# Kernel tuning notes

Hardware: AMD Instinct MI355X
Metric: run time of the kernel (lower is better)

## Reference

```python
import jax, jax.numpy as jnp
import numpy as np
import math

B, H, S, D = 2, 16, 2048, 128

def setup_inputs() -> dict:
    key = jax.random.key(0)
    k1, k2, k3, k4 = jax.random.split(key, 4)
    x1 = jax.random.normal(k1, (B, H, S, D), dtype=jnp.float32)
    x2 = jax.random.normal(k2, (B, H, S, D), dtype=jnp.float32)
    x3 = jax.random.normal(k3, (B, H, D, S), dtype=jnp.float32)
    attn_mask = jax.random.normal(k4, (S, S), dtype=jnp.float32)
    return {"x1": x1, "x2": x2, "x3": x3, "attn_mask": attn_mask}

def reference(x1, x2, x3, attn_mask):
    scale = 1.0 / math.sqrt(x1.shape[-1])
    # [B,H,S,S] scores
    qk = jnp.einsum('bhqd,bhkd->bhqk', x1, x2) * scale + attn_mask
    attn_weight = jax.nn.softmax(qk, axis=-1)
    # x3 @ attn_weight : [B,H,D,S] @ [B,H,S,S] -> [B,H,D,S]
    output = jnp.einsum('bhds,bhsk->bhdk', x3, attn_weight)
    return output
```

## Files before the change

kernel.cpp:

```cpp
#include <hip/hip_runtime.h>


typedef __attribute__((ext_vector_type(8))) short short8;
typedef __attribute__((ext_vector_type(4))) float f32x4;

#define S_LEN 2048
#define D_LEN 128
#define BH_N 32
#define SCALE_QK 0.08838834764831845f

__device__ __forceinline__ unsigned short f2bf(float f) {
    union { float f; unsigned int i; } v; v.f = f;
    unsigned int r = v.i + 0x7FFFu + ((v.i >> 16) & 1u);
    return (unsigned short)(r >> 16);
}
__device__ __forceinline__ float bf2f(unsigned short u) {
    union { unsigned int i; float f; } v; v.i = ((unsigned int)u) << 16; return v.f;
}
__device__ __forceinline__ unsigned pack2bf(float a, float b) {
    unsigned ua = __float_as_uint(a) + 0x8000u;
    unsigned ub = __float_as_uint(b) + 0x8000u;
    return __builtin_amdgcn_perm(ub, ua, 0x07060302);
}
__device__ __forceinline__ uint2 pack4bf(float4 v) {
    uint2 p;
    p.x = pack2bf(v.x, v.y);
    p.y = pack2bf(v.z, v.w);
    return p;
}

__global__ void k_cvt(const float* __restrict__ x1,
                      const float* __restrict__ x2,
                      const float* __restrict__ mask,
                      unsigned short* __restrict__ x1s,
                      unsigned short* __restrict__ x2b,
                      unsigned short* __restrict__ mbf) {
    const size_t N1 = (size_t)BH_N * S_LEN * D_LEN;
    const size_t NM = (size_t)S_LEN * S_LEN;
    size_t i = ((size_t)blockIdx.x * 256 + threadIdx.x) * 4;
    if (i < N1) {
        float4 v = *(const float4*)&x1[i];
        v.x *= SCALE_QK; v.y *= SCALE_QK; v.z *= SCALE_QK; v.w *= SCALE_QK;
        *(uint2*)&x1s[i] = pack4bf(v);
    } else if (i < 2 * N1) {
        size_t j = i - N1;
        float4 v = *(const float4*)&x2[j];
        *(uint2*)&x2b[j] = pack4bf(v);
    } else if (i < 2 * N1 + NM) {
        size_t j = i - 2 * N1;
        float4 v = *(const float4*)&mask[j];
        *(uint2*)&mbf[j] = pack4bf(v);
    }
}

__global__ __launch_bounds__(256, 2) void k_qk(
    const unsigned short* __restrict__ x1s,
    const unsigned short* __restrict__ x2b,
    const unsigned short* __restrict__ mbf,
    const float* __restrict__ x3,
    unsigned short* __restrict__ x3s)
{
    __shared__ unsigned short sK[128 * 128];
    __shared__ float sRL[128];
    const int q0 = blockIdx.x * 128;
    const int bh = blockIdx.y;
    const unsigned short* x1p = x1s + (size_t)bh * S_LEN * D_LEN;
    const unsigned short* x2p = x2b + (size_t)bh * S_LEN * D_LEN;
    const int t = threadIdx.x;
    const int w = t >> 6, lane = t & 63, quad = lane >> 4, l16 = lane & 15;

    short8 aq[2][4];
#pragma unroll
    for (int qb = 0; qb < 2; ++qb)
#pragma unroll
        for (int kk = 0; kk < 4; ++kk)
            aq[qb][kk] = *(const short8*)&x1p[(size_t)(q0 + 32 * w + 16 * qb + l16) * D_LEN
                                              + (kk * 4 + quad) * 8];

    float rs[8] = {0.f, 0.f, 0.f, 0.f, 0.f, 0.f, 0.f, 0.f};

    for (int k0 = 0; k0 < S_LEN; k0 += 128) {
        __syncthreads();
#pragma unroll
        for (int i = 0; i < 8; ++i) {
            int idx = i * 256 + t;
            int r = idx >> 4, c = idx & 15;
            *(uint4*)&sK[r * 128 + ((c ^ (r & 7)) * 8)] =
                *(const uint4*)&x2p[(size_t)(k0 + r) * D_LEN + c * 8];
        }
        __syncthreads();

        f32x4 acc[2][8];
#pragma unroll
        for (int qb = 0; qb < 2; ++qb)
#pragma unroll
            for (int kb = 0; kb < 8; ++kb) acc[qb][kb] = (f32x4){0.f, 0.f, 0.f, 0.f};

#pragma unroll
        for (int kk = 0; kk < 4; ++kk) {
            const int sc = ((kk * 4 + quad) ^ (l16 & 7)) * 8;
            short8 b[8];
#pragma unroll
            for (int kb = 0; kb < 8; ++kb)
                b[kb] = *(const short8*)&sK[(kb * 16 + l16) * 128 + sc];
#pragma unroll
            for (int qb = 0; qb < 2; ++qb)
#pragma unroll
                for (int kb = 0; kb < 8; ++kb)
                    acc[qb][kb] = __builtin_amdgcn_mfma_f32_16x16x32_bf16(aq[qb][kk], b[kb], acc[qb][kb], 0, 0, 0);
        }

#pragma unroll
        for (int qb = 0; qb < 2; ++qb)
#pragma unroll
            for (int kb = 0; kb < 8; ++kb) {
                const size_t mrow = (size_t)(q0 + 32 * w + 16 * qb + 4 * quad) * S_LEN
                                    + k0 + kb * 16 + l16;
#pragma unroll
                for (int rr = 0; rr < 4; ++rr)
                    rs[qb * 4 + rr] += __expf(acc[qb][kb][rr] + bf2f(mbf[mrow + (size_t)rr * S_LEN]));
            }
    }

#pragma unroll
    for (int i = 0; i < 8; ++i) {
        float v = rs[i];
        v += __shfl_xor(v, 1); v += __shfl_xor(v, 2);
        v += __shfl_xor(v, 4); v += __shfl_xor(v, 8);
        if (l16 == 0) sRL[32 * w + 16 * (i >> 2) + 4 * quad + (i & 3)] = 1.0f / v;
    }
    __syncthreads();

    const float* x3b = x3 + (size_t)bh * (size_t)D_LEN * S_LEN;
    unsigned short* x3sp = x3s + (size_t)bh * (size_t)D_LEN * S_LEN;
#pragma unroll
    for (int i = 0; i < 16; ++i) {
        int e = (i * 256 + t) * 4;
        int r = e >> 7, c = e & 127;
        float4 v = *(const float4*)&x3b[(size_t)r * S_LEN + q0 + c];
        v.x *= sRL[c]; v.y *= sRL[c + 1]; v.z *= sRL[c + 2]; v.w *= sRL[c + 3];
        *(uint2*)&x3sp[(size_t)r * S_LEN + q0 + c] = pack4bf(v);
    }
}

__global__ __launch_bounds__(256, 2) void k_out(
    const unsigned short* __restrict__ x1s,
    const unsigned short* __restrict__ x2b,
    const unsigned short* __restrict__ x3s,
    const unsigned short* __restrict__ mbf,
    float* __restrict__ out)
{
    __shared__ unsigned short sK[128 * 128];
    __shared__ unsigned short sQ[64 * 128];
    __shared__ unsigned short sX[128 * 64];
    __shared__ unsigned short sE[128 * 64];
    const int kb0 = blockIdx.x * 128;
    const int bh = blockIdx.y;
    const unsigned short* x1p = x1s + (size_t)bh * S_LEN * D_LEN;
    const unsigned short* x2p = x2b + (size_t)bh * S_LEN * D_LEN;
    const unsigned short* x3p = x3s + (size_t)bh * (size_t)D_LEN * S_LEN;
    const int t = threadIdx.x;
    const int w = t >> 6, lane = t & 63, quad = lane >> 4, l16 = lane & 15;

#pragma unroll
    for (int i = 0; i < 8; ++i) {
        int idx = i * 256 + t;
        int r = idx >> 4, c = idx & 15;
        *(uint4*)&sK[r * 128 + ((c ^ (r & 7)) * 8)] =
            *(const uint4*)&x2p[(size_t)(kb0 + r) * D_LEN + c * 8];
    }

    f32x4 oa[16];
#pragma unroll
    for (int i = 0; i < 16; ++i) oa[i] = (f32x4){0.f, 0.f, 0.f, 0.f};

    __syncthreads();

    short8 bk[2][8];
#pragma unroll
    for (int kk = 0; kk < 2; ++kk) {
        const int sc = ((kk * 4 + quad) ^ (l16 & 7)) * 8;
#pragma unroll
        for (int kb = 0; kb < 8; ++kb)
            bk[kk][kb] = *(const short8*)&sK[(kb * 16 + l16) * 128 + sc];
    }

    for (int q0 = 0; q0 < S_LEN; q0 += 64) {
        __syncthreads();
#pragma unroll
        for (int i = 0; i < 4; ++i) {
            int idx = i * 256 + t;
            int r = idx >> 4, c = idx & 15;
            *(uint4*)&sQ[r * 128 + ((c ^ (r & 7)) * 8)] =
                *(const uint4*)&x1p[(size_t)(q0 + r) * D_LEN + c * 8];
        }
#pragma unroll
        for (int i = 0; i < 4; ++i) {
            int idx = i * 256 + t;
            int r = idx >> 3, c = idx & 7;
            *(uint4*)&sX[r * 64 + ((c ^ (r & 7)) * 8)] =
                *(const uint4*)&x3p[(size_t)r * S_LEN + q0 + c * 8];
        }
        __syncthreads();

        f32x4 acc[8];
#pragma unroll
        for (int kb = 0; kb < 8; ++kb) acc[kb] = (f32x4){0.f, 0.f, 0.f, 0.f};
#pragma unroll
        for (int kk = 0; kk < 2; ++kk) {
            const int sc = ((kk * 4 + quad) ^ (l16 & 7)) * 8;
            short8 a = *(const short8*)&sQ[(16 * w + l16) * 128 + sc];
#pragma unroll
            for (int kb = 0; kb < 8; ++kb)
                acc[kb] = __builtin_amdgcn_mfma_f32_16x16x32_bf16(a, bk[kk][kb], acc[kb], 0, 0, 0);
        }
#pragma unroll
        for (int kk = 2; kk < 4; ++kk) {
            const int sc = ((kk * 4 + quad) ^ (l16 & 7)) * 8;
            short8 a = *(const short8*)&sQ[(16 * w + l16) * 128 + sc];
            short8 b[8];
#pragma unroll
            for (int kb = 0; kb < 8; ++kb)
                b[kb] = *(const short8*)&sK[(kb * 16 + l16) * 128 + sc];
#pragma unroll
            for (int kb = 0; kb < 8; ++kb)
                acc[kb] = __builtin_amdgcn_mfma_f32_16x16x32_bf16(a, b[kb], acc[kb], 0, 0, 0);
        }

        const int qrow = 16 * w + 4 * quad;
        const int qoff7 = qrow & 7;
        const int cE = qrow >> 3;
#pragma unroll
        for (int kb = 0; kb < 8; ++kb) {
            const int kg = kb0 + kb * 16 + l16;
            float e0 = __expf(acc[kb][0] + bf2f(mbf[(size_t)(q0 + qrow + 0) * S_LEN + kg]));
            float e1 = __expf(acc[kb][1] + bf2f(mbf[(size_t)(q0 + qrow + 1) * S_LEN + kg]));
            float e2 = __expf(acc[kb][2] + bf2f(mbf[(size_t)(q0 + qrow + 2) * S_LEN + kg]));
            float e3 = __expf(acc[kb][3] + bf2f(mbf[(size_t)(q0 + qrow + 3) * S_LEN + kg]));
            uint2 pk;
            pk.x = pack2bf(e0, e1);
            pk.y = pack2bf(e2, e3);
            const int krow = kb * 16 + l16;
            *(uint2*)&sE[krow * 64 + ((cE ^ (krow & 7)) * 8) + qoff7] = pk;
        }
        __syncthreads();

#pragma unroll
        for (int kk = 0; kk < 2; ++kk) {
            const int sc = ((kk * 4 + quad) ^ (l16 & 7)) * 8;
            short8 a[2];
#pragma unroll
            for (int db = 0; db < 2; ++db)
                a[db] = *(const short8*)&sX[(32 * w + 16 * db + l16) * 64 + sc];
            short8 b[8];
#pragma unroll
            for (int kb = 0; kb < 8; ++kb)
                b[kb] = *(const short8*)&sE[(kb * 16 + l16) * 64 + sc];
#pragma unroll
            for (int db = 0; db < 2; ++db)
#pragma unroll
                for (int kb = 0; kb < 8; ++kb)
                    oa[db * 8 + kb] = __builtin_amdgcn_mfma_f32_16x16x32_bf16(a[db], b[kb], oa[db * 8 + kb], 0, 0, 0);
        }
    }

#pragma unroll
    for (int db = 0; db < 2; ++db)
#pragma unroll
        for (int kb = 0; kb < 8; ++kb)
#pragma unroll
            for (int rr = 0; rr < 4; ++rr) {
                int d = 32 * w + 16 * db + 4 * quad + rr;
                out[((size_t)bh * D_LEN + d) * S_LEN + kb0 + kb * 16 + l16] =
                    oa[db * 8 + kb][rr];
            }
}

__global__ __launch_bounds__(256, 3) void k_rowsum_fb(
    const float* __restrict__ x1, const float* __restrict__ x2,
    const float* __restrict__ mask, float* __restrict__ rl)
{
    __shared__ unsigned short sQ[128 * 136];
    __shared__ unsigned short sK[64 * 136];
    const int q0 = blockIdx.x * 128;
    const int bh = blockIdx.y;
    const float* x1b = x1 + (size_t)bh * S_LEN * D_LEN;
    const float* x2b = x2 + (size_t)bh * S_LEN * D_LEN;
    const int t = threadIdx.x;
    const int w = t >> 6, lane = t & 63, quad = lane >> 4, l16 = lane & 15;
#pragma unroll
    for (int i = 0; i < 16; ++i) {
        int e = (i * 256 + t) * 4;
        int r = e >> 7, c = e & 127;
        float4 v = *(const float4*)&x1b[(size_t)(q0 + r) * D_LEN + c];
        *(uint2*)&sQ[r * 136 + c] = pack4bf(v);
    }
    float rs[8] = {0.f, 0.f, 0.f, 0.f, 0.f, 0.f, 0.f, 0.f};
    for (int k0 = 0; k0 < S_LEN; k0 += 64) {
        __syncthreads();
#pragma unroll
        for (int i = 0; i < 8; ++i) {
            int e = (i * 256 + t) * 4;
            int r = e >> 7, c = e & 127;
            float4 v = *(const float4*)&x2b[(size_t)(k0 + r) * D_LEN + c];
            *(uint2*)&sK[r * 136 + c] = pack4bf(v);
        }
        __syncthreads();
#pragma unroll
        for (int qb = 0; qb < 2; ++qb) {
            const int qrow = 32 * w + 16 * qb;
#pragma unroll
            for (int kb = 0; kb < 4; ++kb) {
                f32x4 acc = {0.f, 0.f, 0.f, 0.f};
#pragma unroll
                for (int kk = 0; kk < 4; ++kk) {
                    short8 a = *(const short8*)&sQ[(qrow + l16) * 136 + kk * 32 + quad * 8];
                    short8 b = *(const short8*)&sK[(kb * 16 + l16) * 136 + kk * 32 + quad * 8];
                    acc = __builtin_amdgcn_mfma_f32_16x16x32_bf16(a, b, acc, 0, 0, 0);
                }
                const int kg = k0 + kb * 16 + l16;
                const int qg = q0 + qrow + 4 * quad;
#pragma unroll
                for (int r = 0; r < 4; ++r) {
                    float m = mask[(size_t)(qg + r) * S_LEN + kg];
                    rs[qb * 4 + r] += __expf(acc[r] * SCALE_QK + m);
                }
            }
        }
    }
#pragma unroll
    for (int i = 0; i < 8; ++i) {
        float v = rs[i];
        v += __shfl_xor(v, 1); v += __shfl_xor(v, 2);
        v += __shfl_xor(v, 4); v += __shfl_xor(v, 8);
        if (l16 == 0) {
            int qg = q0 + 32 * w + 16 * (i >> 2) + 4 * quad + (i & 3);
            rl[(size_t)bh * S_LEN + qg] = 1.0f / v;
        }
    }
}

__global__ __launch_bounds__(256, 2) void k_out_fb(
    const float* __restrict__ x1, const float* __restrict__ x2,
    const float* __restrict__ x3, const float* __restrict__ mask,
    const float* __restrict__ rl, float* __restrict__ out)
{
    __shared__ unsigned short sK[64 * 136];
    __shared__ unsigned short sQ[64 * 136];
    __shared__ unsigned short sX[128 * 72];
    __shared__ unsigned short sE[64 * 72];
    const int kb0 = blockIdx.x * 64;
    const int bh = blockIdx.y;
    const float* x1b = x1 + (size_t)bh * S_LEN * D_LEN;
    const float* x2b = x2 + (size_t)bh * S_LEN * D_LEN;
    const float* x3b = x3 + (size_t)bh * (size_t)D_LEN * S_LEN;
    const float* rlb = rl + (size_t)bh * S_LEN;
    const int t = threadIdx.x;
    const int w = t >> 6, lane = t & 63, quad = lane >> 4, l16 = lane & 15;
#pragma unroll
    for (int i = 0; i < 8; ++i) {
        int e = (i * 256 + t) * 4;
        int r = e >> 7, c = e & 127;
        float4 v = *(const float4*)&x2b[(size_t)(kb0 + r) * D_LEN + c];
        *(uint2*)&sK[r * 136 + c] = pack4bf(v);
    }
    f32x4 oa[8];
#pragma unroll
    for (int i = 0; i < 8; ++i) oa[i] = (f32x4){0.f, 0.f, 0.f, 0.f};
    for (int q0 = 0; q0 < S_LEN; q0 += 64) {
        __syncthreads();
#pragma unroll
        for (int i = 0; i < 8; ++i) {
            int e = (i * 256 + t) * 4;
            int r = e >> 7, c = e & 127;
            float4 v = *(const float4*)&x1b[(size_t)(q0 + r) * D_LEN + c];
            *(uint2*)&sQ[r * 136 + c] = pack4bf(v);
        }
#pragma unroll
        for (int i = 0; i < 8; ++i) {
            int e = (i * 256 + t) * 4;
            int r = e >> 6, c = e & 63;
            float4 v = *(const float4*)&x3b[(size_t)r * S_LEN + q0 + c];
            *(uint2*)&sX[r * 72 + c] = pack4bf(v);
        }
        __syncthreads();
        const int qrow = 16 * w + 4 * quad;
        float rl4[4];
#pragma unroll
        for (int r = 0; r < 4; ++r) rl4[r] = rlb[q0 + qrow + r];
#pragma unroll
        for (int kb = 0; kb < 4; ++kb) {
            f32x4 acc = {0.f, 0.f, 0.f, 0.f};
#pragma unroll
            for (int kk = 0; kk < 4; ++kk) {
                short8 a = *(const short8*)&sQ[(16 * w + l16) * 136 + kk * 32 + quad * 8];
                short8 b = *(const short8*)&sK[(kb * 16 + l16) * 136 + kk * 32 + quad * 8];
                acc = __builtin_amdgcn_mfma_f32_16x16x32_bf16(a, b, acc, 0, 0, 0);
            }
            const int kg = kb0 + kb * 16 + l16;
            unsigned short e4[4];
#pragma unroll
            for (int r = 0; r < 4; ++r) {
                float m = mask[(size_t)(q0 + qrow + r) * S_LEN + kg];
                e4[r] = f2bf(__expf(acc[r] * SCALE_QK + m) * rl4[r]);
            }
            uint2 pk;
            pk.x = (unsigned)e4[0] | ((unsigned)e4[1] << 16);
            pk.y = (unsigned)e4[2] | ((unsigned)e4[3] << 16);
            *(uint2*)&sE[(kb * 16 + l16) * 72 + qrow] = pk;
        }
        __syncthreads();
#pragma unroll
        for (int db = 0; db < 2; ++db)
#pragma unroll
            for (int kb = 0; kb < 4; ++kb) {
                f32x4 a0 = oa[db * 4 + kb];
#pragma unroll
                for (int kk = 0; kk < 2; ++kk) {
                    short8 a = *(const short8*)&sX[(32 * w + 16 * db + l16) * 72 + kk * 32 + quad * 8];
                    short8 b = *(const short8*)&sE[(kb * 16 + l16) * 72 + kk * 32 + quad * 8];
                    a0 = __builtin_amdgcn_mfma_f32_16x16x32_bf16(a, b, a0, 0, 0, 0);
                }
                oa[db * 4 + kb] = a0;
            }
    }
#pragma unroll
    for (int db = 0; db < 2; ++db)
#pragma unroll
        for (int kb = 0; kb < 4; ++kb)
#pragma unroll
            for (int r = 0; r < 4; ++r) {
                int d = 32 * w + 16 * db + 4 * quad + r;
                out[((size_t)bh * D_LEN + d) * S_LEN + kb0 + kb * 16 + l16] =
                    oa[db * 4 + kb][r];
            }
}

extern "C" void kernel_launch(void* const* d_in, const int* in_sizes, int n_in,
                              void* d_out, int out_size, void* d_ws, size_t ws_size,
                              hipStream_t stream) {
    const float* x1 = (const float*)d_in[0];
    const float* x2 = (const float*)d_in[1];
    const float* x3 = (const float*)d_in[2];
    const float* mask = (const float*)d_in[3];
    float* out = (float*)d_out;

    const size_t N1 = (size_t)BH_N * S_LEN * D_LEN;
    const size_t NM = (size_t)S_LEN * S_LEN;
    const size_t need = (3 * N1 + NM) * sizeof(unsigned short);

    if (ws_size >= need) {
        unsigned short* x1s = (unsigned short*)d_ws;
        unsigned short* x2b = x1s + N1;
        unsigned short* x3s = x2b + N1;
        unsigned short* mbf = x3s + N1;
        const size_t tot4 = (2 * N1 + NM) / 4;
        k_cvt<<<dim3((unsigned)(tot4 / 256)), dim3(256), 0, stream>>>(x1, x2, mask, x1s, x2b, mbf);
        k_qk<<<dim3(S_LEN / 128, BH_N), dim3(256), 0, stream>>>(x1s, x2b, mbf, x3, x3s);
        k_out<<<dim3(S_LEN / 128, BH_N), dim3(256), 0, stream>>>(x1s, x2b, x3s, mbf, out);
    } else {
        float* rl = (float*)d_ws;
        k_rowsum_fb<<<dim3(S_LEN / 128, BH_N), dim3(256), 0, stream>>>(x1, x2, mask, rl);
        k_out_fb<<<dim3(S_LEN / 64, BH_N), dim3(256), 0, stream>>>(x1, x2, x3, mask, rl, out);
    }
}
```

Measured before the change: 322.0 us.

## Halve tile sizes in k_qk and k_out to double grid and raise occupancy

Cuts the query tile in k_qk and the key tile in k_out from 128 to 64 rows, so each kernel launches twice as many blocks (1024 instead of 512 on a 256-CU part) and uses fewer accumulator registers. k_out also shares one LDS buffer between Q and the exp tile, drops the register-cached K fragments, and adds extra barriers to keep that sharing safe. Launch bounds rise so more blocks fit per CU. The cost is less reuse per block: K/Q/X3 tiles and mask reads are repeated across twice as many blocks, and each loop iteration now has more synchronization.

```diff
diff --git a/kernel.cpp b/kernel.cpp
--- a/kernel.cpp
+++ b/kernel.cpp
@@ -53,7 +53,7 @@
     }
 }
 
-__global__ __launch_bounds__(256, 2) void k_qk(
+__global__ __launch_bounds__(256, 4) void k_qk(
     const unsigned short* __restrict__ x1s,
     const unsigned short* __restrict__ x2b,
     const unsigned short* __restrict__ mbf,
@@ -61,23 +61,21 @@
     unsigned short* __restrict__ x3s)
 {
     __shared__ unsigned short sK[128 * 128];
-    __shared__ float sRL[128];
-    const int q0 = blockIdx.x * 128;
+    __shared__ float sRL[64];
+    const int q0 = blockIdx.x * 64;
     const int bh = blockIdx.y;
     const unsigned short* x1p = x1s + (size_t)bh * S_LEN * D_LEN;
     const unsigned short* x2p = x2b + (size_t)bh * S_LEN * D_LEN;
     const int t = threadIdx.x;
     const int w = t >> 6, lane = t & 63, quad = lane >> 4, l16 = lane & 15;
 
-    short8 aq[2][4];
-#pragma unroll
-    for (int qb = 0; qb < 2; ++qb)
-#pragma unroll
-        for (int kk = 0; kk < 4; ++kk)
-            aq[qb][kk] = *(const short8*)&x1p[(size_t)(q0 + 32 * w + 16 * qb + l16) * D_LEN
-                                              + (kk * 4 + quad) * 8];
-
-    float rs[8] = {0.f, 0.f, 0.f, 0.f, 0.f, 0.f, 0.f, 0.f};
+    short8 aq[4];
+#pragma unroll
+    for (int kk = 0; kk < 4; ++kk)
+        aq[kk] = *(const short8*)&x1p[(size_t)(q0 + 16 * w + l16) * D_LEN
+                                       + (kk * 4 + quad) * 8];
+
+    float rs[4] = {0.f, 0.f, 0.f, 0.f};
 
     for (int k0 = 0; k0 < S_LEN; k0 += 128) {
         __syncthreads();
@@ -90,11 +88,9 @@
         }
         __syncthreads();
 
-        f32x4 acc[2][8];
-#pragma unroll
-        for (int qb = 0; qb < 2; ++qb)
-#pragma unroll
-            for (int kb = 0; kb < 8; ++kb) acc[qb][kb] = (f32x4){0.f, 0.f, 0.f, 0.f};
+        f32x4 acc[8];
+#pragma unroll
+        for (int kb = 0; kb < 8; ++kb) acc[kb] = (f32x4){0.f, 0.f, 0.f, 0.f};
 
 #pragma unroll
         for (int kk = 0; kk < 4; ++kk) {
@@ -104,89 +100,78 @@
             for (int kb = 0; kb < 8; ++kb)
                 b[kb] = *(const short8*)&sK[(kb * 16 + l16) * 128 + sc];
 #pragma unroll
-            for (int qb = 0; qb < 2; ++qb)
-#pragma unroll
-                for (int kb = 0; kb < 8; ++kb)
-                    acc[qb][kb] = __builtin_amdgcn_mfma_f32_16x16x32_bf16(aq[qb][kk], b[kb], acc[qb][kb], 0, 0, 0);
-        }
-
-#pragma unroll
-        for (int qb = 0; qb < 2; ++qb)
-#pragma unroll
-            for (int kb = 0; kb < 8; ++kb) {
-                const size_t mrow = (size_t)(q0 + 32 * w + 16 * qb + 4 * quad) * S_LEN
-                                    + k0 + kb * 16 + l16;
-#pragma unroll
-                for (int rr = 0; rr < 4; ++rr)
-                    rs[qb * 4 + rr] += __expf(acc[qb][kb][rr] + bf2f(mbf[mrow + (size_t)rr * S_LEN]));
-            }
-    }
-
-#pragma unroll
-    for (int i = 0; i < 8; ++i) {
+            for (int kb = 0; kb < 8; ++kb)
+                acc[kb] = __builtin_amdgcn_mfma_f32_16x16x32_bf16(aq[kk], b[kb], acc[kb], 0, 0, 0);
+        }
+
+#pragma unroll
+        for (int kb = 0; kb < 8; ++kb) {
+            const size_t mrow = (size_t)(q0 + 16 * w + 4 * quad) * S_LEN
+                                + k0 + kb * 16 + l16;
+#pragma unroll
+            for (int rr = 0; rr < 4; ++rr)
+                rs[rr] += __expf(acc[kb][rr] + bf2f(mbf[mrow + (size_t)rr * S_LEN]));
+        }
+    }
+
+#pragma unroll
+    for (int i = 0; i < 4; ++i) {
         float v = rs[i];
         v += __shfl_xor(v, 1); v += __shfl_xor(v, 2);
         v += __shfl_xor(v, 4); v += __shfl_xor(v, 8);
-        if (l16 == 0) sRL[32 * w + 16 * (i >> 2) + 4 * quad + (i & 3)] = 1.0f / v;
+        if (l16 == 0) sRL[16 * w + 4 * quad + i] = 1.0f / v;
     }
     __syncthreads();
 
     const float* x3b = x3 + (size_t)bh * (size_t)D_LEN * S_LEN;
     unsigned short* x3sp = x3s + (size_t)bh * (size_t)D_LEN * S_LEN;
 #pragma unroll
-    for (int i = 0; i < 16; ++i) {
+    for (int i = 0; i < 8; ++i) {
         int e = (i * 256 + t) * 4;
-        int r = e >> 7, c = e & 127;
+        int r = e >> 6, c = e & 63;
         float4 v = *(const float4*)&x3b[(size_t)r * S_LEN + q0 + c];
         v.x *= sRL[c]; v.y *= sRL[c + 1]; v.z *= sRL[c + 2]; v.w *= sRL[c + 3];
         *(uint2*)&x3sp[(size_t)r * S_LEN + q0 + c] = pack4bf(v);
     }
 }
 
-__global__ __launch_bounds__(256, 2) void k_out(
+__global__ __launch_bounds__(256, 3) void k_out(
     const unsigned short* __restrict__ x1s,
     const unsigned short* __restrict__ x2b,
     const unsigned short* __restrict__ x3s,
     const unsigned short* __restrict__ mbf,
     float* __restrict__ out)
 {
-    __shared__ unsigned short sK[128 * 128];
+    __shared__ unsigned short sK[64 * 128];
     __shared__ unsigned short sQ[64 * 128];
     __shared__ unsigned short sX[128 * 64];
-    __shared__ unsigned short sE[128 * 64];
-    const int kb0 = blockIdx.x * 128;
+    unsigned short* sE = sQ;
+    const int kb0 = blockIdx.x * 64;
     const int bh = blockIdx.y;
     const unsigned short* x1p = x1s + (size_t)bh * S_LEN * D_LEN;
     const unsigned short* x2p = x2b + (size_t)bh * S_LEN * D_LEN;
     const unsigned short* x3p = x3s + (size_t)bh * (size_t)D_LEN * S_LEN;
     const int t = threadIdx.x;
     const int w = t >> 6, lane = t & 63, quad = lane >> 4, l16 = lane & 15;
-
-#pragma unroll
-    for (int i = 0; i < 8; ++i) {
+    const int qrow = 16 * w + 4 * quad;
+    const int cE = qrow >> 3;
+    const int qoff7 = qrow & 7;
+
+#pragma unroll
+    for (int i = 0; i < 4; ++i) {
         int idx = i * 256 + t;
         int r = idx >> 4, c = idx & 15;
         *(uint4*)&sK[r * 128 + ((c ^ (r & 7)) * 8)] =
             *(const uint4*)&x2p[(size_t)(kb0 + r) * D_LEN + c * 8];
     }
 
-    f32x4 oa[16];
-#pragma unroll
-    for (int i = 0; i < 16; ++i) oa[i] = (f32x4){0.f, 0.f, 0.f, 0.f};
+    f32x4 oa[8];
+#pragma unroll
+    for (int i = 0; i < 8; ++i) oa[i] = (f32x4){0.f, 0.f, 0.f, 0.f};
 
     __syncthreads();
 
-    short8 bk[2][8];
-#pragma unroll
-    for (int kk = 0; kk < 2; ++kk) {
-        const int sc = ((kk * 4 + quad) ^ (l16 & 7)) * 8;
-#pragma unroll
-        for (int kb = 0; kb < 8; ++kb)
-            bk[kk][kb] = *(const short8*)&sK[(kb * 16 + l16) * 128 + sc];
-    }
-
     for (int q0 = 0; q0 < S_LEN; q0 += 64) {
-        __syncthreads();
 #pragma unroll
         for (int i = 0; i < 4; ++i) {
             int idx = i * 256 + t;
@@ -203,45 +188,39 @@
         }
         __syncthreads();
 
-        f32x4 acc[8];
-#pragma unroll
-        for (int kb = 0; kb < 8; ++kb) acc[kb] = (f32x4){0.f, 0.f, 0.f, 0.f};
-#pragma unroll
-        for (int kk = 0; kk < 2; ++kk) {
+        f32x4 acc[4];
+#pragma unroll
+        for (int kb = 0; kb < 4; ++kb) acc[kb] = (f32x4){0.f, 0.f, 0.f, 0.f};
+#pragma unroll
+        for (int kk = 0; kk < 4; ++kk) {
             const int sc = ((kk * 4 + quad) ^ (l16 & 7)) * 8;
             short8 a = *(const short8*)&sQ[(16 * w + l16) * 128 + sc];
-#pragma unroll
-            for (int kb = 0; kb < 8; ++kb)
-                acc[kb] = __builtin_amdgcn_mfma_f32_16x16x32_bf16(a, bk[kk][kb], acc[kb], 0, 0, 0);
-        }
-#pragma unroll
-        for (int kk = 2; kk < 4; ++kk) {
-            const int sc = ((kk * 4 + quad) ^ (l16 & 7)) * 8;
-            short8 a = *(const short8*)&sQ[(16 * w + l16) * 128 + sc];
-            short8 b[8];
-#pragma unroll
-            for (int kb = 0; kb < 8; ++kb)
+            short8 b[4];
+#pragma unroll
+            for (int kb = 0; kb < 4; ++kb)
                 b[kb] = *(const short8*)&sK[(kb * 16 + l16) * 128 + sc];
 #pragma unroll
-            for (int kb = 0; kb < 8; ++kb)
+            for (int kb = 0; kb < 4; ++kb)
                 acc[kb] = __builtin_amdgcn_mfma_f32_16x16x32_bf16(a, b[kb], acc[kb], 0, 0, 0);
         }
 
-        const int qrow = 16 * w + 4 * quad;
-        const int qoff7 = qrow & 7;
-        const int cE = qrow >> 3;
-#pragma unroll
-        for (int kb = 0; kb < 8; ++kb) {
+        uint2 pk[4];
+#pragma unroll
+        for (int kb = 0; kb < 4; ++kb) {
             const int kg = kb0 + kb * 16 + l16;
             float e0 = __expf(acc[kb][0] + bf2f(mbf[(size_t)(q0 + qrow + 0) * S_LEN + kg]));
             float e1 = __expf(acc[kb][1] + bf2f(mbf[(size_t)(q0 + qrow + 1) * S_LEN + kg]));
             float e2 = __expf(acc[kb][2] + bf2f(mbf[(size_t)(q0 + qrow + 2) * S_LEN + kg]));
             float e3 = __expf(acc[kb][3] + bf2f(mbf[(size_t)(q0 + qrow + 3) * S_LEN + kg]));
-            uint2 pk;
-            pk.x = pack2bf(e0, e1);
-            pk.y = pack2bf(e2, e3);
+            pk[kb].x = pack2bf(e0, e1);
+            pk[kb].y = pack2bf(e2, e3);
+        }
+
+        __syncthreads();
+#pragma unroll
+        for (int kb = 0; kb < 4; ++kb) {
             const int krow = kb * 16 + l16;
-            *(uint2*)&sE[krow * 64 + ((cE ^ (krow & 7)) * 8) + qoff7] = pk;
+            *(uint2*)&sE[krow * 64 + ((cE ^ (krow & 7)) * 8) + qoff7] = pk[kb];
         }
         __syncthreads();
 
@@ -252,27 +231,28 @@
 #pragma unroll
             for (int db = 0; db < 2; ++db)
                 a[db] = *(const short8*)&sX[(32 * w + 16 * db + l16) * 64 + sc];
-            short8 b[8];
-#pragma unroll
-            for (int kb = 0; kb < 8; ++kb)
+            short8 b[4];
+#pragma unroll
+            for (int kb = 0; kb < 4; ++kb)
                 b[kb] = *(const short8*)&sE[(kb * 16 + l16) * 64 + sc];
 #pragma unroll
             for (int db = 0; db < 2; ++db)
 #pragma unroll
-                for (int kb = 0; kb < 8; ++kb)
-                    oa[db * 8 + kb] = __builtin_amdgcn_mfma_f32_16x16x32_bf16(a[db], b[kb], oa[db * 8 + kb], 0, 0, 0);
-        }
+                for (int kb = 0; kb < 4; ++kb)
+                    oa[db * 4 + kb] = __builtin_amdgcn_mfma_f32_16x16x32_bf16(a[db], b[kb], oa[db * 4 + kb], 0, 0, 0);
+        }
+        __syncthreads();
     }
 
 #pragma unroll
     for (int db = 0; db < 2; ++db)
 #pragma unroll
-        for (int kb = 0; kb < 8; ++kb)
+        for (int kb = 0; kb < 4; ++kb)
 #pragma unroll
             for (int rr = 0; rr < 4; ++rr) {
                 int d = 32 * w + 16 * db + 4 * quad + rr;
                 out[((size_t)bh * D_LEN + d) * S_LEN + kb0 + kb * 16 + l16] =
-                    oa[db * 8 + kb][rr];
+                    oa[db * 4 + kb][rr];
             }
 }
 
@@ -456,8 +436,8 @@
         unsigned short* mbf = x3s + N1;
         const size_t tot4 = (2 * N1 + NM) / 4;
         k_cvt<<<dim3((unsigned)(tot4 / 256)), dim3(256), 0, stream>>>(x1, x2, mask, x1s, x2b, mbf);
-        k_qk<<<dim3(S_LEN / 128, BH_N), dim3(256), 0, stream>>>(x1s, x2b, mbf, x3, x3s);
-        k_out<<<dim3(S_LEN / 128, BH_N), dim3(256), 0, stream>>>(x1s, x2b, x3s, mbf, out);
+        k_qk<<<dim3(S_LEN / 64, BH_N), dim3(256), 0, stream>>>(x1s, x2b, mbf, x3, x3s);
+        k_out<<<dim3(S_LEN / 64, BH_N), dim3(256), 0, stream>>>(x1s, x2b, x3s, mbf, out);
     } else {
         float* rl = (float*)d_ws;
         k_rowsum_fb<<<dim3(S_LEN / 128, BH_N), dim3(256), 0, stream>>>(x1, x2, mask, rl);
```

Measured after the change: 387.4 us. +20.3%, slower.
